# Optimization experiments

Hardware: AMD Instinct MI355X
Metric: run time of the kernel (lower is better)

## Reference

```python
import jax, jax.numpy as jnp
import numpy as np

N = 16384          # num nodes
E = 262144         # num edges (before self loops)
IN_DIM = 128
HID = 128
OUT = 2
TRIM = 0.1
MAX_DEG = 48       # padded max in-degree (incl. self loop); safe bound for Poisson(16)+1
BN_EPS = 1e-5


def _lin_params(key, fan_in, fan_out):
    kw, kb = jax.random.split(key)
    s = 1.0 / np.sqrt(fan_in)
    W = jax.random.uniform(kw, (fan_in, fan_out), jnp.float32, -s, s)
    b = jax.random.uniform(kb, (fan_out,), jnp.float32, -s, s)
    return W, b


def setup_inputs() -> dict:
    key = jax.random.key(0)
    ks = jax.random.split(key, 8)
    x = jax.random.normal(ks[0], (N, IN_DIM), jnp.float32)
    edge_index = jax.random.randint(ks[1], (2, E), 0, N, jnp.int32)
    Wl0, bl0 = _lin_params(ks[2], IN_DIM, HID)
    Wr0, br0 = _lin_params(ks[3], IN_DIM, HID)
    Wl1, bl1 = _lin_params(ks[4], HID, HID)
    Wr1, br1 = _lin_params(ks[5], HID, HID)
    Wl2, bl2 = _lin_params(ks[6], HID, OUT)
    Wr2, br2 = _lin_params(ks[7], HID, OUT)
    g0 = jnp.ones((HID,), jnp.float32); be0 = jnp.zeros((HID,), jnp.float32)
    g1 = jnp.ones((HID,), jnp.float32); be1 = jnp.zeros((HID,), jnp.float32)
    return dict(x=x, edge_index=edge_index,
                Wl0=Wl0, bl0=bl0, Wr0=Wr0, br0=br0, g0=g0, be0=be0,
                Wl1=Wl1, bl1=bl1, Wr1=Wr1, br1=br1, g1=g1, be1=be1,
                Wl2=Wl2, bl2=bl2, Wr2=Wr2, br2=br2)


def _forward(edge_index, x, Wl0, bl0, Wr0, br0, g0, be0,
             Wl1, bl1, Wr1, br1, g1, be1, Wl2, bl2, Wr2, br2):
    loops = jnp.arange(N, dtype=edge_index.dtype)
    row = jnp.concatenate([edge_index[0], loops])   # source nodes
    col = jnp.concatenate([edge_index[1], loops])   # destination nodes
    counts = jax.ops.segment_sum(jnp.ones_like(col), col, num_segments=N)  # in-degree, int
    deg = jnp.maximum(counts, 1).astype(x.dtype)
    norm = 1.0 / deg[col]                            # 1/deg(dst), per edge

    # Edge ordering grouped by destination node; rank = slot within the node's group.
    perm = jnp.argsort(col, stable=True)
    col_s = col[perm]
    starts = jnp.cumsum(counts) - counts
    rank = jnp.arange(col.shape[0], dtype=counts.dtype) - starts[col_s]
    node_id = jnp.where(rank < MAX_DEG, col_s, N)    # overflow slots -> OOB, dropped by scatter

    t = jnp.maximum(1, jnp.floor(counts.astype(jnp.float32) * TRIM).astype(counts.dtype))
    tcnt = counts - 2 * t
    pos = jnp.arange(MAX_DEG)[None, :]
    sel = (pos >= t[:, None]) & (pos < (counts - t)[:, None])   # [N, MAX_DEG]
    use_trim = (counts >= 5) & (tcnt > 0)
    inv_tcnt = 1.0 / jnp.maximum(tcnt, 1).astype(x.dtype)

    def trimmed_scatter(msg):
        # plain mean fallback
        mean = jax.ops.segment_sum(msg, col, num_segments=N) / deg[:, None]
        d = msg.shape[1]
        # padded per-node buffer; +inf pads sort to the end (never selected by `sel`)
        dense = jnp.full((N, MAX_DEG, d), jnp.inf, msg.dtype)
        dense = dense.at[node_id, rank].set(msg[perm], mode='drop')
        sdense = jnp.sort(dense, axis=1)             # per-feature sort within each node
        tmean = jnp.sum(jnp.where(sel[:, :, None], sdense, 0.0), axis=1) * inv_tcnt[:, None]
        return jnp.where(use_trim[:, None], tmean, mean)

    def conv(h, Wl, bl, Wr, br):
        msg = (h @ Wl + bl)[row] * norm[:, None]
        return trimmed_scatter(msg) + h @ Wr + br

    bn_scale = jnp.float32(1.0 / np.sqrt(1.0 + BN_EPS))  # eval-mode BN: running mean 0, var 1
    h = conv(x, Wl0, bl0, Wr0, br0)
    h = jax.nn.relu(h * bn_scale * g0 + be0)
    h = conv(h, Wl1, bl1, Wr1, br1)
    h = jax.nn.relu(h * bn_scale * g1 + be1)
    return conv(h, Wl2, bl2, Wr2, br2)


def reference(x, edge_index, Wl0, bl0, Wr0, br0, g0, be0,
              Wl1, bl1, Wr1, br1, g1, be1, Wl2, bl2, Wr2, br2):
    return _forward(edge_index, x, Wl0, bl0, Wr0, br0, g0, be0,
                    Wl1, bl1, Wr1, br1, g1, be1, Wl2, bl2, Wr2, br2)
```

## Files before the change

### kernel.cpp

```cpp
#include <hip/hip_runtime.h>
#include <hip/hip_fp16.h>
#include <math.h>

#define GN    16384
#define MAXD  48
#define BN_SCALE 0.9999950000374998f

typedef __attribute__((ext_vector_type(8))) short short8;
typedef __attribute__((ext_vector_type(4))) float f32x4;
typedef _Float16 __attribute__((ext_vector_type(2))) h2v;

__device__ inline short f2bf(float x) {
    unsigned u = __float_as_uint(x);
    return (short)((u + 0x7fffu + ((u >> 16) & 1u)) >> 16);
}
__device__ inline float bf2f(short s) {
    return __uint_as_float(((unsigned)(unsigned short)s) << 16);
}

struct F2 { float x, y; };
__device__ inline F2 f2min(F2 a, F2 b) { return {fminf(a.x, b.x), fminf(a.y, b.y)}; }
__device__ inline F2 f2max(F2 a, F2 b) { return {fmaxf(a.x, b.x), fmaxf(a.y, b.y)}; }

__device__ inline F2 trim_core(const _Float16* __restrict__ HL,
                               const int* __restrict__ srow, int cnt, int d, int f2i)
{
    F2 tot = {0.f, 0.f};
    F2 s0 = { INFINITY,  INFINITY}, s1 = s0, s2 = s0, s3 = s0;
    F2 l0 = {-INFINITY, -INFINITY}, l1 = l0, l2 = l0, l3 = l0;

    if (cnt < 20) {
        int i = 0;
        for (; i + 8 <= d; i += 8) {
            h2v b[8];
            #pragma unroll
            for (int k = 0; k < 8; ++k)
                b[k] = *reinterpret_cast<const h2v*>(HL + srow[i + k] + f2i);
            #pragma unroll
            for (int k = 0; k < 8; ++k) {
                F2 x = {(float)b[k][0], (float)b[k][1]};
                tot.x += x.x; tot.y += x.y;
                s0 = f2min(s0, x);
                l0 = f2max(l0, x);
            }
        }
        for (; i < d; ++i) {
            h2v hv = *reinterpret_cast<const h2v*>(HL + srow[i] + f2i);
            F2 x = {(float)hv[0], (float)hv[1]};
            tot.x += x.x; tot.y += x.y;
            s0 = f2min(s0, x);
            l0 = f2max(l0, x);
        }
    } else {
        int i = 0;
        for (; i + 8 <= d; i += 8) {
            h2v b[8];
            #pragma unroll
            for (int k = 0; k < 8; ++k)
                b[k] = *reinterpret_cast<const h2v*>(HL + srow[i + k] + f2i);
            #pragma unroll
            for (int k = 0; k < 8; ++k) {
                F2 x = {(float)b[k][0], (float)b[k][1]};
                tot.x += x.x; tot.y += x.y;
                F2 a = x;
                F2 t0 = f2min(s0, a); a = f2max(s0, a); s0 = t0;
                F2 t1 = f2min(s1, a); a = f2max(s1, a); s1 = t1;
                F2 t2 = f2min(s2, a); a = f2max(s2, a); s2 = t2;
                s3 = f2min(s3, a);
                F2 bb = x;
                F2 u0 = f2max(l0, bb); bb = f2min(l0, bb); l0 = u0;
                F2 u1 = f2max(l1, bb); bb = f2min(l1, bb); l1 = u1;
                F2 u2 = f2max(l2, bb); bb = f2min(l2, bb); l2 = u2;
                l3 = f2max(l3, bb);
            }
        }
        for (; i < d; ++i) {
            h2v hv = *reinterpret_cast<const h2v*>(HL + srow[i] + f2i);
            F2 x = {(float)hv[0], (float)hv[1]};
            tot.x += x.x; tot.y += x.y;
            F2 a = x;
            F2 t0 = f2min(s0, a); a = f2max(s0, a); s0 = t0;
            F2 t1 = f2min(s1, a); a = f2max(s1, a); s1 = t1;
            F2 t2 = f2min(s2, a); a = f2max(s2, a); s2 = t2;
            s3 = f2min(s3, a);
            F2 bb = x;
            F2 u0 = f2max(l0, bb); bb = f2min(l0, bb); l0 = u0;
            F2 u1 = f2max(l1, bb); bb = f2min(l1, bb); l1 = u1;
            F2 u2 = f2max(l2, bb); bb = f2min(l2, bb); l2 = u2;
            l3 = f2max(l3, bb);
        }
    }

    int t = (int)floorf((float)cnt * 0.1f);
    if (t < 1) t = 1;
    int tcnt = cnt - 2 * t;
    bool use_trim = (cnt >= 5) && (tcnt > 0);
    float dd = (float)cnt;
    F2 res;
    if (use_trim) {
        int tt = min(t, 4);
        F2 bot = s0, top = l0;
        if (tt > 1) { bot.x += s1.x; bot.y += s1.y; top.x += l1.x; top.y += l1.y; }
        if (tt > 2) { bot.x += s2.x; bot.y += s2.y; top.x += l2.x; top.y += l2.y; }
        if (tt > 3) { bot.x += s3.x; bot.y += s3.y; top.x += l3.x; top.y += l3.y; }
        float inv = 1.0f / (dd * (float)tcnt);
        res.x = (tot.x - bot.x - top.x) * inv;
        res.y = (tot.y - bot.y - top.y) * inv;
    } else {
        float inv = 1.0f / (dd * dd);
        res.x = tot.x * inv;
        res.y = tot.y * inv;
    }
    return res;
}

__global__ __launch_bounds__(256) void k_prep(
    int* __restrict__ fill,
    const float* __restrict__ Wl0, const float* __restrict__ Wr0,
    const float* __restrict__ Wl1, const float* __restrict__ Wr1,
    short* __restrict__ W5)
{
    int t = blockIdx.x * 256 + threadIdx.x;
    fill[t] = 0;

    int layer = t >> 13;
    int g     = t & 8191;
    int split = (g >> 12) & 1;
    int ks    = (g >> 10) & 3;
    int nt    = (g >> 6) & 15;
    int l     = g & 63;
    int q = l >> 4, r = l & 15;
    int n = nt * 16 + r;
    const float* W = (n < 128) ? (layer ? Wl1 : Wl0) : (layer ? Wr1 : Wr0);
    int ncol = n & 127;
    short8 o8;
    #pragma unroll
    for (int j = 0; j < 8; ++j) {
        int k = ks * 32 + (j >> 2) * 16 + q * 4 + (j & 3);
        float wv = W[k * 128 + ncol];
        short hi = f2bf(wv);
        o8[j] = split ? f2bf(wv - bf2f(hi)) : hi;
    }
    *reinterpret_cast<short8*>(W5 + ((size_t)layer * 8192 + g) * 8) = o8;
}

template<int NT>
__device__ inline void gemm_tile_t(const short8 Ahi[4], const short8 Alo[4],
                                   const short* __restrict__ W5,
                                   const float* __restrict__ bl,
                                   const float* __restrict__ br,
                                   _Float16* __restrict__ HL, float* __restrict__ HR,
                                   int tile, int half, int ntg0, int q, int r, int l)
{
    f32x4 acc[NT];
    #pragma unroll
    for (int nt = 0; nt < NT; ++nt) {
        int ntg = ntg0 + nt;
        float b = (ntg < 8) ? bl[ntg * 16 + r] : br[(ntg - 8) * 16 + r];
        acc[nt] = (f32x4){b, b, b, b};
    }
    #pragma unroll
    for (int ks = 0; ks < 4; ++ks) {
        #pragma unroll
        for (int nt = 0; nt < NT; ++nt) {
            int ntg = ntg0 + nt;
            short8 Bhi = *reinterpret_cast<const short8*>(
                W5 + ((size_t)(ks * 16 + ntg) * 64 + l) * 8);
            short8 Blo = *reinterpret_cast<const short8*>(
                W5 + ((size_t)((4 + ks) * 16 + ntg) * 64 + l) * 8);
            acc[nt] = __builtin_amdgcn_mfma_f32_16x16x32_bf16(Ahi[ks], Bhi, acc[nt], 0, 0, 0);
            acc[nt] = __builtin_amdgcn_mfma_f32_16x16x32_bf16(Ahi[ks], Blo, acc[nt], 0, 0, 0);
            acc[nt] = __builtin_amdgcn_mfma_f32_16x16x32_bf16(Alo[ks], Bhi, acc[nt], 0, 0, 0);
        }
    }
    const int rb = tile * 32 + half * 16 + 4 * q;
    #pragma unroll
    for (int nt = 0; nt < NT; ++nt) {
        int ntg = ntg0 + nt;
        if (ntg < 8) {
            int c = ntg * 16 + r;
            #pragma unroll
            for (int j = 0; j < 4; ++j)
                HL[(size_t)(rb + j) * 128 + c] = (_Float16)acc[nt][j];
        } else {
            int c = (ntg - 8) * 16 + r;
            #pragma unroll
            for (int j = 0; j < 4; ++j)
                HR[(size_t)(rb + j) * 128 + c] = acc[nt][j];
        }
    }
}

__global__ __launch_bounds__(512, 4) void k_fused0(
    const float* __restrict__ X, const int* __restrict__ ei, int E,
    int* __restrict__ adj, int* __restrict__ fill,
    const short* __restrict__ W5,
    const float* __restrict__ bl, const float* __restrict__ br,
    _Float16* __restrict__ HL, float* __restrict__ HR)
{
    const int tid = threadIdx.x;
    if (blockIdx.x >= 512) {
        const int* src = ei;
        const int* dst = ei + E;
        int g0 = (blockIdx.x - 512) * 512 + tid;
        for (int i = g0; i < E + GN; i += 64 * 512) {
            int s, dv;
            if (i < E) { s = src[i]; dv = dst[i]; }
            else       { s = i - E;  dv = i - E; }
            int slot = atomicAdd(&fill[dv], 1);
            if (slot < MAXD) adj[dv * MAXD + slot] = s;
        }
        return;
    }
    const int w = tid >> 6, l = tid & 63;
    const int q = l >> 4, r = l & 15;
    const int half = w & 1, quarter = w >> 1;
    const int rowA = blockIdx.x * 32 + half * 16 + r;

    short8 Ahi[4], Alo[4];
    const float4* xp = reinterpret_cast<const float4*>(X + (size_t)rowA * 128);
    #pragma unroll
    for (int h = 0; h < 8; ++h) {
        float4 v = xp[h * 4 + q];
        float xv[4] = {v.x, v.y, v.z, v.w};
        int ks = h >> 1, hk = h & 1;
        #pragma unroll
        for (int j = 0; j < 4; ++j) {
            short hi = f2bf(xv[j]);
            Ahi[ks][hk * 4 + j] = hi;
            Alo[ks][hk * 4 + j] = f2bf(xv[j] - bf2f(hi));
        }
    }
    gemm_tile_t<4>(Ahi, Alo, W5, bl, br, HL, HR, blockIdx.x, half, quarter * 4, q, r, l);
}

__global__ __launch_bounds__(512, 4) void k_fused1(
    const _Float16* __restrict__ HL0, const float* __restrict__ HR0,
    const int* __restrict__ adj, const int* __restrict__ fill,
    const float* __restrict__ g, const float* __restrict__ be,
    const short* __restrict__ W5,
    const float* __restrict__ bl, const float* __restrict__ br,
    _Float16* __restrict__ HL1, float* __restrict__ HR1)
{
    __shared__ float hbs[32][132];
    __shared__ int sadj[8][MAXD];
    const int tid = threadIdx.x, w = tid >> 6, l = tid & 63;
    const int f2i = l * 2;
    const int v0 = blockIdx.x * 32;

    for (int s = 0; s < 4; ++s) {
        const int v = v0 + w * 4 + s;
        const int cnt = fill[v];
        const int d = min(cnt, MAXD);
        if (l < d) sadj[w][l] = adj[v * MAXD + l] * 128;
        F2 res = trim_core(HL0, sadj[w], cnt, d, f2i);
        const float2 hrv = *reinterpret_cast<const float2*>(HR0 + (size_t)v * 128 + f2i);
        hbs[w * 4 + s][f2i]     = fmaxf((res.x + hrv.x) * (BN_SCALE * g[f2i])     + be[f2i],     0.f);
        hbs[w * 4 + s][f2i + 1] = fmaxf((res.y + hrv.y) * (BN_SCALE * g[f2i + 1]) + be[f2i + 1], 0.f);
    }
    __syncthreads();

    const int q = l >> 4, r = l & 15;
    const int half = w & 1, quarter = w >> 1;
    const int m = half * 16 + r;
    short8 Ahi[4], Alo[4];
    #pragma unroll
    for (int h = 0; h < 8; ++h) {
        float4 vv = *reinterpret_cast<const float4*>(&hbs[m][h * 16 + 4 * q]);
        float xv[4] = {vv.x, vv.y, vv.z, vv.w};
        int ks = h >> 1, hk = h & 1;
        #pragma unroll
        for (int j = 0; j < 4; ++j) {
            short hi = f2bf(xv[j]);
            Ahi[ks][hk * 4 + j] = hi;
            Alo[ks][hk * 4 + j] = f2bf(xv[j] - bf2f(hi));
        }
    }
    gemm_tile_t<4>(Ahi, Alo, W5, bl, br, HL1, HR1, blockIdx.x, half, quarter * 4, q, r, l);
}

__global__ __launch_bounds__(256) void k_fused2(
    const _Float16* __restrict__ HL1, const float* __restrict__ HR1,
    const int* __restrict__ adj, const int* __restrict__ fill,
    const float* __restrict__ g, const float* __restrict__ be,
    const float* __restrict__ Wl2, const float* __restrict__ bl2,
    const float* __restrict__ Wr2, const float* __restrict__ br2,
    float* __restrict__ hl2, float* __restrict__ hr2)
{
    __shared__ int sadj[4][MAXD];
    const int tid = threadIdx.x, w = tid >> 6, l = tid & 63;
    const int f2i = l * 2;
    const int v = blockIdx.x * 4 + w;
    const int cnt = fill[v];
    const int d = min(cnt, MAXD);
    if (l < d) sadj[w][l] = adj[v * MAXD + l] * 128;
    F2 res = trim_core(HL1, sadj[w], cnt, d, f2i);
    const float2 hrv = *reinterpret_cast<const float2*>(HR1 + (size_t)v * 128 + f2i);
    float h0 = fmaxf((res.x + hrv.x) * (BN_SCALE * g[f2i])     + be[f2i],     0.f);
    float h1 = fmaxf((res.y + hrv.y) * (BN_SCALE * g[f2i + 1]) + be[f2i + 1], 0.f);

    float4 wl = *reinterpret_cast<const float4*>(Wl2 + l * 4);
    float4 wr = *reinterpret_cast<const float4*>(Wr2 + l * 4);
    float p0 = h0 * wl.x + h1 * wl.z;
    float p1 = h0 * wl.y + h1 * wl.w;
    float p2 = h0 * wr.x + h1 * wr.z;
    float p3 = h0 * wr.y + h1 * wr.w;
    #pragma unroll
    for (int off = 1; off < 64; off <<= 1) {
        p0 += __shfl_xor(p0, off);
        p1 += __shfl_xor(p1, off);
        p2 += __shfl_xor(p2, off);
        p3 += __shfl_xor(p3, off);
    }
    if (l == 0) {
        hl2[v * 2 + 0] = p0 + bl2[0];
        hl2[v * 2 + 1] = p1 + bl2[1];
        hr2[v * 2 + 0] = p2 + br2[0];
        hr2[v * 2 + 1] = p3 + br2[1];
    }
}

__global__ __launch_bounds__(256) void k_agg_out(
    const float* __restrict__ hl2, const float* __restrict__ hr2,
    const int* __restrict__ adj, const int* __restrict__ fill,
    float* __restrict__ out)
{
    int idx = blockIdx.x * 256 + threadIdx.x;
    int v = idx >> 1, j = idx & 1;
    int cnt = fill[v];
    int d = min(cnt, MAXD);
    const int* ap = adj + v * MAXD;

    float total = 0.f;
    float s0 = INFINITY, s1 = INFINITY, s2 = INFINITY, s3 = INFINITY;
    float l0 = -INFINITY, l1 = -INFINITY, l2 = -INFINITY, l3 = -INFINITY;
    int i = 0;
    for (; i + 8 <= d; i += 8) {
        float b[8];
        #pragma unroll
        for (int k = 0; k < 8; ++k) b[k] = hl2[ap[i + k] * 2 + j];
        #pragma unroll
        for (int k = 0; k < 8; ++k) {
            float x = b[k];
            total += x;
            float a = x;
            float t0 = fminf(s0, a); a = fmaxf(s0, a); s0 = t0;
            float t1 = fminf(s1, a); a = fmaxf(s1, a); s1 = t1;
            float t2 = fminf(s2, a); a = fmaxf(s2, a); s2 = t2;
            s3 = fminf(s3, a);
            float bb = x;
            float u0 = fmaxf(l0, bb); bb = fminf(l0, bb); l0 = u0;
            float u1 = fmaxf(l1, bb); bb = fminf(l1, bb); l1 = u1;
            float u2 = fmaxf(l2, bb); bb = fminf(l2, bb); l2 = u2;
            l3 = fmaxf(l3, bb);
        }
    }
    for (; i < d; ++i) {
        float x = hl2[ap[i] * 2 + j];
        total += x;
        float a = x;
        float t0 = fminf(s0, a); a = fmaxf(s0, a); s0 = t0;
        float t1 = fminf(s1, a); a = fmaxf(s1, a); s1 = t1;
        float t2 = fminf(s2, a); a = fmaxf(s2, a); s2 = t2;
        s3 = fminf(s3, a);
        float bb = x;
        float u0 = fmaxf(l0, bb); bb = fminf(l0, bb); l0 = u0;
        float u1 = fmaxf(l1, bb); bb = fminf(l1, bb); l1 = u1;
        float u2 = fmaxf(l2, bb); bb = fminf(l2, bb); l2 = u2;
        l3 = fmaxf(l3, bb);
    }

    int t = (int)floorf((float)cnt * 0.1f);
    if (t < 1) t = 1;
    int tcnt = cnt - 2 * t;
    bool use_trim = (cnt >= 5) && (tcnt > 0);
    float dd = (float)cnt;
    float res;
    if (use_trim) {
        int tt = min(t, 4);
        float bot = s0, top = l0;
        if (tt > 1) { bot += s1; top += l1; }
        if (tt > 2) { bot += s2; top += l2; }
        if (tt > 3) { bot += s3; top += l3; }
        res = (total - bot - top) / (dd * (float)tcnt);
    } else {
        res = total / (dd * dd);
    }
    out[idx] = res + hr2[idx];
}

extern "C" void kernel_launch(void* const* d_in, const int* in_sizes, int n_in,
                              void* d_out, int out_size, void* d_ws, size_t ws_size,
                              hipStream_t stream)
{
    const float* x   = (const float*)d_in[0];
    const int*   ei  = (const int*)d_in[1];
    const int    E   = in_sizes[1] / 2;
    const float* Wl0 = (const float*)d_in[2];
    const float* bl0 = (const float*)d_in[3];
    const float* Wr0 = (const float*)d_in[4];
    const float* br0 = (const float*)d_in[5];
    const float* g0  = (const float*)d_in[6];
    const float* be0 = (const float*)d_in[7];
    const float* Wl1 = (const float*)d_in[8];
    const float* bl1 = (const float*)d_in[9];
    const float* Wr1 = (const float*)d_in[10];
    const float* br1 = (const float*)d_in[11];
    const float* g1  = (const float*)d_in[12];
    const float* be1 = (const float*)d_in[13];
    const float* Wl2 = (const float*)d_in[14];
    const float* bl2 = (const float*)d_in[15];
    const float* Wr2 = (const float*)d_in[16];
    const float* br2 = (const float*)d_in[17];
    float* out = (float*)d_out;

    char* w = (char*)d_ws;
    int*      adj  = (int*)w;       w += (size_t)GN * MAXD * 4;
    int*      fill = (int*)w;       w += (size_t)GN * 4;
    _Float16* HL0  = (_Float16*)w;  w += (size_t)GN * 128 * 2;
    float*    HR0  = (float*)w;     w += (size_t)GN * 128 * 4;
    _Float16* HL1  = (_Float16*)w;  w += (size_t)GN * 128 * 2;
    float*    HR1  = (float*)w;     w += (size_t)GN * 128 * 4;
    short*    W5   = (short*)w;     w += (size_t)2 * 8192 * 16;
    float*    hl2  = (float*)w;     w += (size_t)GN * 2 * 4;
    float*    hr2  = (float*)w;     w += (size_t)GN * 2 * 4;

    k_prep  <<<GN / 256, 256, 0, stream>>>(fill, Wl0, Wr0, Wl1, Wr1, W5);
    k_fused0<<<576, 512, 0, stream>>>(x, ei, E, adj, fill, W5, bl0, br0, HL0, HR0);
    k_fused1<<<GN / 32, 512, 0, stream>>>(HL0, HR0, adj, fill, g0, be0,
                                          W5 + (size_t)8192 * 8, bl1, br1, HL1, HR1);
    k_fused2<<<GN / 4, 256, 0, stream>>>(HL1, HR1, adj, fill, g1, be1,
                                         Wl2, bl2, Wr2, br2, hl2, hr2);
    k_agg_out<<<GN * 2 / 256, 256, 0, stream>>>(hl2, hr2, adj, fill, out);
}
```

Before: 179.0 us.

## Interleave two-node trimmed aggregation and predicate gather tails with nontemporal hints

Rewrites the trimmed-mean gather loop to process full 8-wide batches with clamped indices and validity masks, which removes the scalar remainder loop. In the layer-1 fused kernel each wave now aggregates two nodes at once so more independent gathers are in flight. Nontemporal loads and stores are added for X, HR0, HR1 and the HR writes to reduce cache pollution. In exchange, padded lanes issue redundant loads, register pressure rises, and the light path is taken only when both nodes qualify.

```diff
diff --git a/kernel.cpp b/kernel.cpp
--- a/kernel.cpp
+++ b/kernel.cpp
@@ -8,6 +8,8 @@
 
 typedef __attribute__((ext_vector_type(8))) short short8;
 typedef __attribute__((ext_vector_type(4))) float f32x4;
+typedef __attribute__((ext_vector_type(2))) float f32x2v;
+typedef __attribute__((ext_vector_type(4))) float f32x4v;
 typedef _Float16 __attribute__((ext_vector_type(2))) h2v;
 
 __device__ inline short f2bf(float x) {
@@ -22,75 +24,37 @@
 __device__ inline F2 f2min(F2 a, F2 b) { return {fminf(a.x, b.x), fminf(a.y, b.y)}; }
 __device__ inline F2 f2max(F2 a, F2 b) { return {fmaxf(a.x, b.x), fmaxf(a.y, b.y)}; }
 
-__device__ inline F2 trim_core(const _Float16* __restrict__ HL,
-                               const int* __restrict__ srow, int cnt, int d, int f2i)
-{
-    F2 tot = {0.f, 0.f};
-    F2 s0 = { INFINITY,  INFINITY}, s1 = s0, s2 = s0, s3 = s0;
-    F2 l0 = {-INFINITY, -INFINITY}, l1 = l0, l2 = l0, l3 = l0;
-
-    if (cnt < 20) {
-        int i = 0;
-        for (; i + 8 <= d; i += 8) {
-            h2v b[8];
-            #pragma unroll
-            for (int k = 0; k < 8; ++k)
-                b[k] = *reinterpret_cast<const h2v*>(HL + srow[i + k] + f2i);
-            #pragma unroll
-            for (int k = 0; k < 8; ++k) {
-                F2 x = {(float)b[k][0], (float)b[k][1]};
-                tot.x += x.x; tot.y += x.y;
-                s0 = f2min(s0, x);
-                l0 = f2max(l0, x);
-            }
-        }
-        for (; i < d; ++i) {
-            h2v hv = *reinterpret_cast<const h2v*>(HL + srow[i] + f2i);
-            F2 x = {(float)hv[0], (float)hv[1]};
-            tot.x += x.x; tot.y += x.y;
-            s0 = f2min(s0, x);
-            l0 = f2max(l0, x);
-        }
-    } else {
-        int i = 0;
-        for (; i + 8 <= d; i += 8) {
-            h2v b[8];
-            #pragma unroll
-            for (int k = 0; k < 8; ++k)
-                b[k] = *reinterpret_cast<const h2v*>(HL + srow[i + k] + f2i);
-            #pragma unroll
-            for (int k = 0; k < 8; ++k) {
-                F2 x = {(float)b[k][0], (float)b[k][1]};
-                tot.x += x.x; tot.y += x.y;
-                F2 a = x;
-                F2 t0 = f2min(s0, a); a = f2max(s0, a); s0 = t0;
-                F2 t1 = f2min(s1, a); a = f2max(s1, a); s1 = t1;
-                F2 t2 = f2min(s2, a); a = f2max(s2, a); s2 = t2;
-                s3 = f2min(s3, a);
-                F2 bb = x;
-                F2 u0 = f2max(l0, bb); bb = f2min(l0, bb); l0 = u0;
-                F2 u1 = f2max(l1, bb); bb = f2min(l1, bb); l1 = u1;
-                F2 u2 = f2max(l2, bb); bb = f2min(l2, bb); l2 = u2;
-                l3 = f2max(l3, bb);
-            }
-        }
-        for (; i < d; ++i) {
-            h2v hv = *reinterpret_cast<const h2v*>(HL + srow[i] + f2i);
-            F2 x = {(float)hv[0], (float)hv[1]};
-            tot.x += x.x; tot.y += x.y;
-            F2 a = x;
-            F2 t0 = f2min(s0, a); a = f2max(s0, a); s0 = t0;
-            F2 t1 = f2min(s1, a); a = f2max(s1, a); s1 = t1;
-            F2 t2 = f2min(s2, a); a = f2max(s2, a); s2 = t2;
-            s3 = f2min(s3, a);
-            F2 bb = x;
-            F2 u0 = f2max(l0, bb); bb = f2min(l0, bb); l0 = u0;
-            F2 u1 = f2max(l1, bb); bb = f2min(l1, bb); l1 = u1;
-            F2 u2 = f2max(l2, bb); bb = f2min(l2, bb); l2 = u2;
-            l3 = f2max(l3, bb);
-        }
-    }
-
+struct Trk {
+    F2 tot, s0, s1, s2, s3, l0, l1, l2, l3;
+};
+__device__ inline void trk_init(Trk& T) {
+    T.tot = {0.f, 0.f};
+    T.s0 = T.s1 = T.s2 = T.s3 = { INFINITY,  INFINITY};
+    T.l0 = T.l1 = T.l2 = T.l3 = {-INFINITY, -INFINITY};
+}
+__device__ inline void trk_push_light(Trk& T, F2 x, bool valid) {
+    F2 xs = {valid ? x.x :  INFINITY, valid ? x.y :  INFINITY};
+    F2 xl = {valid ? x.x : -INFINITY, valid ? x.y : -INFINITY};
+    T.tot.x += valid ? x.x : 0.f;
+    T.tot.y += valid ? x.y : 0.f;
+    T.s0 = f2min(T.s0, xs);
+    T.l0 = f2max(T.l0, xl);
+}
+__device__ inline void trk_push_full(Trk& T, F2 x, bool valid) {
+    F2 a = {valid ? x.x :  INFINITY, valid ? x.y :  INFINITY};
+    F2 b = {valid ? x.x : -INFINITY, valid ? x.y : -INFINITY};
+    T.tot.x += valid ? x.x : 0.f;
+    T.tot.y += valid ? x.y : 0.f;
+    F2 t0 = f2min(T.s0, a); a = f2max(T.s0, a); T.s0 = t0;
+    F2 t1 = f2min(T.s1, a); a = f2max(T.s1, a); T.s1 = t1;
+    F2 t2 = f2min(T.s2, a); a = f2max(T.s2, a); T.s2 = t2;
+    T.s3 = f2min(T.s3, a);
+    F2 u0 = f2max(T.l0, b); b = f2min(T.l0, b); T.l0 = u0;
+    F2 u1 = f2max(T.l1, b); b = f2min(T.l1, b); T.l1 = u1;
+    F2 u2 = f2max(T.l2, b); b = f2min(T.l2, b); T.l2 = u2;
+    T.l3 = f2max(T.l3, b);
+}
+__device__ inline F2 trk_finish(const Trk& T, int cnt) {
     int t = (int)floorf((float)cnt * 0.1f);
     if (t < 1) t = 1;
     int tcnt = cnt - 2 * t;
@@ -99,19 +63,44 @@
     F2 res;
     if (use_trim) {
         int tt = min(t, 4);
-        F2 bot = s0, top = l0;
-        if (tt > 1) { bot.x += s1.x; bot.y += s1.y; top.x += l1.x; top.y += l1.y; }
-        if (tt > 2) { bot.x += s2.x; bot.y += s2.y; top.x += l2.x; top.y += l2.y; }
-        if (tt > 3) { bot.x += s3.x; bot.y += s3.y; top.x += l3.x; top.y += l3.y; }
+        F2 bot = T.s0, top = T.l0;
+        if (tt > 1) { bot.x += T.s1.x; bot.y += T.s1.y; top.x += T.l1.x; top.y += T.l1.y; }
+        if (tt > 2) { bot.x += T.s2.x; bot.y += T.s2.y; top.x += T.l2.x; top.y += T.l2.y; }
+        if (tt > 3) { bot.x += T.s3.x; bot.y += T.s3.y; top.x += T.l3.x; top.y += T.l3.y; }
         float inv = 1.0f / (dd * (float)tcnt);
-        res.x = (tot.x - bot.x - top.x) * inv;
-        res.y = (tot.y - bot.y - top.y) * inv;
+        res.x = (T.tot.x - bot.x - top.x) * inv;
+        res.y = (T.tot.y - bot.y - top.y) * inv;
     } else {
         float inv = 1.0f / (dd * dd);
-        res.x = tot.x * inv;
-        res.y = tot.y * inv;
+        res.x = T.tot.x * inv;
+        res.y = T.tot.y * inv;
     }
     return res;
+}
+
+__device__ inline F2 trim_core(const _Float16* __restrict__ HL,
+                               const int* __restrict__ srow, int cnt, int d, int f2i)
+{
+    Trk T; trk_init(T);
+    bool light = (cnt < 20);
+    for (int i = 0; i < d; i += 8) {
+        h2v b[8];
+        #pragma unroll
+        for (int k = 0; k < 8; ++k) {
+            int ia = min(i + k, d - 1);
+            b[k] = *reinterpret_cast<const h2v*>(HL + srow[ia] + f2i);
+        }
+        if (light) {
+            #pragma unroll
+            for (int k = 0; k < 8; ++k)
+                trk_push_light(T, {(float)b[k][0], (float)b[k][1]}, i + k < d);
+        } else {
+            #pragma unroll
+            for (int k = 0; k < 8; ++k)
+                trk_push_full(T, {(float)b[k][0], (float)b[k][1]}, i + k < d);
+        }
+    }
+    return trk_finish(T, cnt);
 }
 
 __global__ __launch_bounds__(256) void k_prep(
@@ -186,7 +175,7 @@
             int c = (ntg - 8) * 16 + r;
             #pragma unroll
             for (int j = 0; j < 4; ++j)
-                HR[(size_t)(rb + j) * 128 + c] = acc[nt][j];
+                __builtin_nontemporal_store(acc[nt][j], &HR[(size_t)(rb + j) * 128 + c]);
         }
     }
 }
@@ -218,10 +207,10 @@
     const int rowA = blockIdx.x * 32 + half * 16 + r;
 
     short8 Ahi[4], Alo[4];
-    const float4* xp = reinterpret_cast<const float4*>(X + (size_t)rowA * 128);
+    const f32x4v* xp = reinterpret_cast<const f32x4v*>(X + (size_t)rowA * 128);
     #pragma unroll
     for (int h = 0; h < 8; ++h) {
-        float4 v = xp[h * 4 + q];
+        f32x4v v = __builtin_nontemporal_load(xp + h * 4 + q);
         float xv[4] = {v.x, v.y, v.z, v.w};
         int ks = h >> 1, hk = h & 1;
         #pragma unroll
@@ -243,20 +232,58 @@
     _Float16* __restrict__ HL1, float* __restrict__ HR1)
 {
     __shared__ float hbs[32][132];
-    __shared__ int sadj[8][MAXD];
+    __shared__ int sadj[8][2][MAXD];
     const int tid = threadIdx.x, w = tid >> 6, l = tid & 63;
     const int f2i = l * 2;
     const int v0 = blockIdx.x * 32;
-
-    for (int s = 0; s < 4; ++s) {
-        const int v = v0 + w * 4 + s;
-        const int cnt = fill[v];
-        const int d = min(cnt, MAXD);
-        if (l < d) sadj[w][l] = adj[v * MAXD + l] * 128;
-        F2 res = trim_core(HL0, sadj[w], cnt, d, f2i);
-        const float2 hrv = *reinterpret_cast<const float2*>(HR0 + (size_t)v * 128 + f2i);
-        hbs[w * 4 + s][f2i]     = fmaxf((res.x + hrv.x) * (BN_SCALE * g[f2i])     + be[f2i],     0.f);
-        hbs[w * 4 + s][f2i + 1] = fmaxf((res.y + hrv.y) * (BN_SCALE * g[f2i + 1]) + be[f2i + 1], 0.f);
+    const float gs0 = BN_SCALE * g[f2i], gs1 = BN_SCALE * g[f2i + 1];
+    const float be0 = be[f2i], be1 = be[f2i + 1];
+
+    for (int p = 0; p < 2; ++p) {
+        const int vA = v0 + w * 4 + p * 2;
+        const int vB = vA + 1;
+        const int cA = fill[vA], cB = fill[vB];
+        const int dA = min(cA, MAXD), dB = min(cB, MAXD);
+        if (l < dA) sadj[w][0][l] = adj[vA * MAXD + l] * 128;
+        if (l < dB) sadj[w][1][l] = adj[vB * MAXD + l] * 128;
+
+        Trk TA, TB;
+        trk_init(TA); trk_init(TB);
+        const bool light = (cA < 20) && (cB < 20);
+        const int dmax = max(dA, dB);
+        for (int i = 0; i < dmax; i += 8) {
+            h2v bA[8], bB[8];
+            #pragma unroll
+            for (int k = 0; k < 8; ++k) {
+                int iaA = min(i + k, dA - 1);
+                int iaB = min(i + k, dB - 1);
+                bA[k] = *reinterpret_cast<const h2v*>(HL0 + sadj[w][0][iaA] + f2i);
+                bB[k] = *reinterpret_cast<const h2v*>(HL0 + sadj[w][1][iaB] + f2i);
+            }
+            if (light) {
+                #pragma unroll
+                for (int k = 0; k < 8; ++k) {
+                    trk_push_light(TA, {(float)bA[k][0], (float)bA[k][1]}, i + k < dA);
+                    trk_push_light(TB, {(float)bB[k][0], (float)bB[k][1]}, i + k < dB);
+                }
+            } else {
+                #pragma unroll
+                for (int k = 0; k < 8; ++k) {
+                    trk_push_full(TA, {(float)bA[k][0], (float)bA[k][1]}, i + k < dA);
+                    trk_push_full(TB, {(float)bB[k][0], (float)bB[k][1]}, i + k < dB);
+                }
+            }
+        }
+        F2 rA = trk_finish(TA, cA);
+        F2 rB = trk_finish(TB, cB);
+        const f32x2v hrA = __builtin_nontemporal_load(
+            reinterpret_cast<const f32x2v*>(HR0 + (size_t)vA * 128 + f2i));
+        const f32x2v hrB = __builtin_nontemporal_load(
+            reinterpret_cast<const f32x2v*>(HR0 + (size_t)vB * 128 + f2i));
+        hbs[w * 4 + p * 2][f2i]         = fmaxf((rA.x + hrA.x) * gs0 + be0, 0.f);
+        hbs[w * 4 + p * 2][f2i + 1]     = fmaxf((rA.y + hrA.y) * gs1 + be1, 0.f);
+        hbs[w * 4 + p * 2 + 1][f2i]     = fmaxf((rB.x + hrB.x) * gs0 + be0, 0.f);
+        hbs[w * 4 + p * 2 + 1][f2i + 1] = fmaxf((rB.y + hrB.y) * gs1 + be1, 0.f);
     }
     __syncthreads();
 
@@ -295,7 +322,8 @@
     const int d = min(cnt, MAXD);
     if (l < d) sadj[w][l] = adj[v * MAXD + l] * 128;
     F2 res = trim_core(HL1, sadj[w], cnt, d, f2i);
-    const float2 hrv = *reinterpret_cast<const float2*>(HR1 + (size_t)v * 128 + f2i);
+    const f32x2v hrv = __builtin_nontemporal_load(
+        reinterpret_cast<const f32x2v*>(HR1 + (size_t)v * 128 + f2i));
     float h0 = fmaxf((res.x + hrv.x) * (BN_SCALE * g[f2i])     + be[f2i],     0.f);
     float h1 = fmaxf((res.y + hrv.y) * (BN_SCALE * g[f2i + 1]) + be[f2i + 1], 0.f);
 
@@ -334,40 +362,31 @@
     float total = 0.f;
     float s0 = INFINITY, s1 = INFINITY, s2 = INFINITY, s3 = INFINITY;
     float l0 = -INFINITY, l1 = -INFINITY, l2 = -INFINITY, l3 = -INFINITY;
-    int i = 0;
-    for (; i + 8 <= d; i += 8) {
+    for (int i = 0; i < d; i += 8) {
         float b[8];
-        #pragma unroll
-        for (int k = 0; k < 8; ++k) b[k] = hl2[ap[i + k] * 2 + j];
+        bool val[8];
         #pragma unroll
         for (int k = 0; k < 8; ++k) {
-            float x = b[k];
-            total += x;
-            float a = x;
+            int ia = min(i + k, d - 1);
+            b[k] = hl2[ap[ia] * 2 + j];
+            val[k] = (i + k) < d;
+        }
+        #pragma unroll
+        for (int k = 0; k < 8; ++k) {
+            float xs = val[k] ? b[k] :  INFINITY;
+            float xl = val[k] ? b[k] : -INFINITY;
+            total += val[k] ? b[k] : 0.f;
+            float a = xs;
             float t0 = fminf(s0, a); a = fmaxf(s0, a); s0 = t0;
             float t1 = fminf(s1, a); a = fmaxf(s1, a); s1 = t1;
             float t2 = fminf(s2, a); a = fmaxf(s2, a); s2 = t2;
             s3 = fminf(s3, a);
-            float bb = x;
+            float bb = xl;
             float u0 = fmaxf(l0, bb); bb = fminf(l0, bb); l0 = u0;
             float u1 = fmaxf(l1, bb); bb = fminf(l1, bb); l1 = u1;
             float u2 = fmaxf(l2, bb); bb = fminf(l2, bb); l2 = u2;
             l3 = fmaxf(l3, bb);
         }
-    }
-    for (; i < d; ++i) {
-        float x = hl2[ap[i] * 2 + j];
-        total += x;
-        float a = x;
-        float t0 = fminf(s0, a); a = fmaxf(s0, a); s0 = t0;
-        float t1 = fminf(s1, a); a = fmaxf(s1, a); s1 = t1;
-        float t2 = fminf(s2, a); a = fmaxf(s2, a); s2 = t2;
-        s3 = fminf(s3, a);
-        float bb = x;
-        float u0 = fmaxf(l0, bb); bb = fminf(l0, bb); l0 = u0;
-        float u1 = fmaxf(l1, bb); bb = fminf(l1, bb); l1 = u1;
-        float u2 = fmaxf(l2, bb); bb = fminf(l2, bb); l2 = u2;
-        l3 = fmaxf(l3, bb);
     }
 
     int t = (int)floorf((float)cnt * 0.1f);
```

Result: slower. 193.7 us (+8.2%).
